# Kernel tuning notes

Measured on AMD Instinct MI355X. Metric: run time of the kernel, lower is better.

The kernel has to match this reference:

```python
import jax, jax.numpy as jnp
import numpy as np

V, B, C, H, W, D, G = 5, 1, 32, 384, 384, 4, 8


def _rot(a, b, c):
    ca, sa = np.cos(a), np.sin(a)
    cb, sb = np.cos(b), np.sin(b)
    cc, sc = np.cos(c), np.sin(c)
    Rx = np.array([[1, 0, 0], [0, ca, -sa], [0, sa, ca]])
    Ry = np.array([[cb, 0, sb], [0, 1, 0], [-sb, 0, cb]])
    Rz = np.array([[cc, -sc, 0], [sc, cc, 0], [0, 0, 1]])
    return (Rz @ Ry @ Rx).astype(np.float32)


def setup_inputs():
    key = jax.random.key(0)
    ks = jax.random.split(key, 8)
    features = jax.random.normal(ks[0], (V, B, C, H, W), jnp.float32)
    current_depths = jax.random.uniform(ks[1], (B, D, H, W), jnp.float32, 425.0, 935.0)
    rng = np.random.RandomState(0)
    Ks = np.zeros((B, V, 3, 3), np.float32)
    Es = np.zeros((B, V, 3, 4), np.float32)
    for b in range(B):
        for v in range(V):
            f = 0.8 * W * (1.0 + 0.01 * rng.randn())
            Ks[b, v] = np.array([[f, 0, W / 2.0], [0, f, H / 2.0], [0, 0, 1.0]], np.float32)
            if v == 0:
                Rm = np.eye(3, dtype=np.float32)
                t = np.zeros(3, np.float32)
            else:
                Rm = _rot(*(0.02 * rng.randn(3)))
                t = np.array([25.0 * v, 5.0 * rng.randn(), 5.0 * rng.randn()], np.float32)
            Es[b, v, :, :3] = Rm
            Es[b, v, :, 3] = t
    w0 = 0.3 * jax.random.normal(ks[2], (16, G), jnp.float32)
    b0 = jnp.zeros((16,), jnp.float32)
    w1 = 0.3 * jax.random.normal(ks[3], (8, 16), jnp.float32)
    b1 = jnp.zeros((8,), jnp.float32)
    w2 = 0.3 * jax.random.normal(ks[4], (1, 8), jnp.float32)
    b2 = jnp.zeros((1,), jnp.float32)
    return {"features": features, "current_depths": current_depths,
            "cam_intrinsic": jnp.asarray(Ks), "cam_extrinsic": jnp.asarray(Es),
            "w0": w0, "b0": b0, "w1": w1, "b1": b1, "w2": w2, "b2": b2}


def _bilinear_sample(feat, px, py):
    # feat [B,C,H,W]; px,py [B,N] pixel coords (align_corners=True), zero padding
    Bn, Cn, Hn, Wn = feat.shape
    ff = feat.reshape(Bn, Cn, Hn * Wn)
    x0 = jnp.floor(px)
    y0 = jnp.floor(py)
    wx1 = px - x0
    wx0 = 1.0 - wx1
    wy1 = py - y0
    wy0 = 1.0 - wy1

    def gather(xi, yi, w):
        valid = (xi >= 0) & (xi <= Wn - 1) & (yi >= 0) & (yi <= Hn - 1)
        xc = jnp.clip(xi, 0, Wn - 1).astype(jnp.int32)
        yc = jnp.clip(yi, 0, Hn - 1).astype(jnp.int32)
        idx = yc * Wn + xc  # [B,N]
        v = jnp.take_along_axis(ff, idx[:, None, :], axis=2)  # [B,C,N]
        return v * (w * valid)[:, None, :]

    return (gather(x0, y0, wx0 * wy0) + gather(x0 + 1.0, y0, wx1 * wy0)
            + gather(x0, y0 + 1.0, wx0 * wy1) + gather(x0 + 1.0, y0 + 1.0, wx1 * wy1))


def _pixelwise_net(sim, w0, b0, w1, b1, w2, b2):
    # PixelwiseNet: 1x1x1 Conv3d G->16->8->1 (BN folded to identity, eval stats), sigmoid, max over depth
    x = jax.nn.relu(jnp.einsum('og,bgdhw->bodhw', w0, sim) + b0[None, :, None, None, None])
    x = jax.nn.relu(jnp.einsum('oc,bcdhw->bodhw', w1, x) + b1[None, :, None, None, None])
    x = jnp.einsum('oc,bcdhw->bodhw', w2, x) + b2[None, :, None, None, None]
    return jnp.max(jax.nn.sigmoid(x), axis=2)  # [B,1,H,W]


def reference(features, current_depths, cam_intrinsic, cam_extrinsic, w0, b0, w1, b1, w2, b2):
    ref_feat = features[0]                                   # [B,C,H,W]
    ref_g = ref_feat.reshape(B, G, C // G, H, W)
    # pixel grid with half-pixel centers, homogeneous [3, H*W]
    xs = jnp.arange(W, dtype=jnp.float32) + 0.5
    ys = jnp.arange(H, dtype=jnp.float32) + 0.5
    gx, gy = jnp.meshgrid(xs, ys)                            # [H,W]
    grid = jnp.stack([gx.ravel(), gy.ravel(), jnp.ones(H * W, jnp.float32)], 0)
    K_ref_inv = jnp.linalg.inv(cam_intrinsic[:, 0])          # [B,3,3]
    R = cam_extrinsic[:, :, :3, :3]                          # [B,V,3,3]
    t = cam_extrinsic[:, :, :3, 3:4]                         # [B,V,3,1]
    R_ref_inv = jnp.linalg.inv(R[:, 0])                      # [B,3,3]
    uv = jnp.einsum('bij,jn->bin', K_ref_inv, grid)          # [B,3,HW]
    cam_pts = uv[:, None] * current_depths.reshape(B, D, 1, H * W)   # [B,D,3,HW]
    world = jnp.einsum('bij,bdjn->bdin', R_ref_inv, cam_pts - t[:, 0:1])
    world = world.transpose(0, 2, 1, 3).reshape(B, 3, D * H * W)     # [B,3,N], N=D*H*W
    sim_sum = 0.0
    w_sum = 0.0
    for s in range(1, V):
        cp = jnp.einsum('bij,bjn->bin', R[:, s], world) + t[:, s]    # [B,3,N]
        uvd = jnp.einsum('bij,bjn->bin', cam_intrinsic[:, s], cp)
        z = uvd[:, 2] + 1e-9
        px = uvd[:, 0] / z
        py = uvd[:, 1] / z
        warped = _bilinear_sample(features[s], px, py)               # [B,C,N]
        warped = warped.reshape(B, G, C // G, D, H, W)
        sim = jnp.mean(warped * ref_g[:, :, :, None], axis=2)        # [B,G,D,H,W]
        vw = _pixelwise_net(sim, w0, b0, w1, b1, w2, b2)             # [B,1,H,W]
        sim_sum = sim_sum + sim * vw[:, :, None]
        w_sum = w_sum + vw[:, :, None]
    return sim_sum / w_sum
```

## Files before the change

kernel.cpp:

```cpp
#include <hip/hip_runtime.h>
#include <math.h>

#define Vn 5
#define Cn 32
#define Hn 384
#define Wn 384
#define Dn 4
#define Gn 8
#define HWn (Hn*Wn)

typedef _Float16 h2 __attribute__((ext_vector_type(2)));
typedef float    f2 __attribute__((ext_vector_type(2)));

__device__ __forceinline__ float fdot2h(h2 a, h2 b, float c){
#if __has_builtin(__builtin_amdgcn_fdot2)
    return __builtin_amdgcn_fdot2(a, b, c, false);
#else
    return (float)a.x*(float)b.x + (float)a.y*(float)b.y + c;
#endif
}
__device__ __forceinline__ unsigned int packh2(float a, float b){
    h2 h;
    h.x = (_Float16)a;
    h.y = (_Float16)b;
    return __builtin_bit_cast(unsigned int, h);
}
__device__ __forceinline__ f2 fma2(f2 a, f2 b, f2 c){ return __builtin_elementwise_fma(a, b, c); }
__device__ __forceinline__ f2 max2(f2 a, f2 b){ return __builtin_elementwise_max(a, b); }
__device__ __forceinline__ f2 splat2(float x){ f2 r; r.x = x; r.y = x; return r; }

__device__ __forceinline__ void inv3(const float* m, float* o){
    float a=m[0],b=m[1],c=m[2],d=m[3],e=m[4],f=m[5],g=m[6],h=m[7],i=m[8];
    float A =  e*i - f*h;
    float B = -(d*i - f*g);
    float C =  d*h - e*g;
    float det = a*A + b*B + c*C;
    float r = 1.f/det;
    o[0] = A*r;            o[1] = -(b*i - c*h)*r;  o[2] =  (b*f - c*e)*r;
    o[3] = B*r;            o[4] =  (a*i - c*g)*r;  o[5] = -(a*f - c*d)*r;
    o[6] = C*r;            o[7] = -(a*h - b*g)*r;  o[8] =  (a*e - b*d)*r;
}
__device__ __forceinline__ void mm3(const float* a, const float* b, float* o){
    #pragma unroll
    for (int r=0;r<3;r++)
        #pragma unroll
        for (int c=0;c<3;c++)
            o[r*3+c] = a[r*3+0]*b[0*3+c] + a[r*3+1]*b[1*3+c] + a[r*3+2]*b[2*3+c];
}
__device__ __forceinline__ void mv3(const float* a, const float* v, float* o){
    #pragma unroll
    for (int r=0;r<3;r++)
        o[r] = a[r*3+0]*v[0] + a[r*3+1]*v[1] + a[r*3+2]*v[2];
}

__global__ __launch_bounds__(256)
void transpose_kernel(const float* __restrict__ feat, unsigned short* __restrict__ featT){
    const int s  = blockIdx.y;
    const int p0 = blockIdx.x * 1024 + threadIdx.x * 4;
    const float* src = feat + (size_t)(s+1)*Cn*HWn + p0;
    unsigned int outw[4][16];
    #pragma unroll
    for (int c=0; c<Cn; c+=2){
        const float4 a = *(const float4*)(src + (size_t)c*HWn);
        const float4 b = *(const float4*)(src + (size_t)(c+1)*HWn);
        outw[0][c>>1] = packh2(a.x, b.x);
        outw[1][c>>1] = packh2(a.y, b.y);
        outw[2][c>>1] = packh2(a.z, b.z);
        outw[3][c>>1] = packh2(a.w, b.w);
    }
    uint4* dst = (uint4*)(featT + ((size_t)s*HWn + p0)*Cn);
    #pragma unroll
    for (int p=0;p<4;p++){
        #pragma unroll
        for (int q=0;q<4;q++){
            uint4 o;
            o.x = outw[p][4*q+0];
            o.y = outw[p][4*q+1];
            o.z = outw[p][4*q+2];
            o.w = outw[p][4*q+3];
            dst[p*4+q] = o;
        }
    }
}

#define DOTG(uA, uB, g, WV)                                                    \
    {                                                                          \
        const h2 pa = __builtin_bit_cast(h2, (uA));                            \
        const h2 pb = __builtin_bit_cast(h2, (uB));                            \
        const float dt = fdot2h(pa, r2[2*(g)], fdot2h(pb, r2[2*(g)+1], 0.f));  \
        sg[(g)] = fmaf((WV), dt, sg[(g)]);                                     \
    }

__device__ __forceinline__ void tap_f16(const unsigned short* __restrict__ vbase,
                                        int xc, int yc, float w,
                                        const h2* r2, float* sg)
{
    if (w != 0.f){
        const uint4* p = (const uint4*)(vbase + ((size_t)yc*Wn + xc)*Cn);
        const uint4 q0 = p[0];
        const uint4 q1 = p[1];
        const uint4 q2 = p[2];
        const uint4 q3 = p[3];
        DOTG(q0.x, q0.y, 0, w)
        DOTG(q0.z, q0.w, 1, w)
        DOTG(q1.x, q1.y, 2, w)
        DOTG(q1.z, q1.w, 3, w)
        DOTG(q2.x, q2.y, 4, w)
        DOTG(q2.z, q2.w, 5, w)
        DOTG(q3.x, q3.y, 6, w)
        DOTG(q3.z, q3.w, 7, w)
    }
}

__global__ __launch_bounds__(256, 2)
void gbinet_kernel(const float* __restrict__ feat,
                   const float* __restrict__ depths,
                   const float* __restrict__ Kin,
                   const float* __restrict__ Ein,
                   const float* __restrict__ w0, const float* __restrict__ b0,
                   const float* __restrict__ w1, const float* __restrict__ b1,
                   const float* __restrict__ w2, const float* __restrict__ b2,
                   const unsigned short* __restrict__ featT,
                   float* __restrict__ out)
{
    __shared__ float sW0[128], sW1[128], sB0[16], sB1[8], sW2[8], sB2s[1];
    __shared__ float sM[48];
    __shared__ float sRef[64*33];
    __shared__ float sDep[4*65];
    __shared__ float sOut[64*33];
    const int t = threadIdx.x;
    if (t < 128){ sW0[t] = w0[t]; sW1[t] = w1[t]; }
    if (t < 16) sB0[t] = b0[t];
    if (t < 8){ sB1[t] = b1[t]; sW2[t] = w2[t]; }

    const int bid = blockIdx.x;
    const int sid = (bid & 7) * (HWn/64/8) + (bid >> 3);
    const int blockBase = sid * 64;

    {
        const float* srcR = feat + blockBase;
        #pragma unroll
        for (int k=0;k<8;k++){
            const int i  = k*256 + t;
            const int c  = i >> 6;
            const int px = i & 63;
            sRef[px*33 + c] = srcR[(size_t)c*HWn + px];
        }
        const int dp = t >> 6;
        const int px = t & 63;
        sDep[dp*65 + px] = depths[(size_t)dp*HWn + blockBase + px];
    }

    if (t < 4){
        float K0inv[9]; inv3(Kin, K0inv);
        float R0[9], t0[3];
        #pragma unroll
        for (int r=0;r<3;r++){
            #pragma unroll
            for (int c=0;c<3;c++) R0[r*3+c] = Ein[r*4+c];
            t0[r] = Ein[r*4+3];
        }
        float R0inv[9]; inv3(R0, R0inv);
        float M0[9]; mm3(R0inv, K0inv, M0);
        float Rt0[3]; mv3(R0inv, t0, Rt0);
        const int sv = t + 1;
        const float* Ks = Kin + sv*9;
        const float* Es = Ein + sv*12;
        float Rs[9], ts[3];
        #pragma unroll
        for (int r=0;r<3;r++){
            #pragma unroll
            for (int c=0;c<3;c++) Rs[r*3+c] = Es[r*4+c];
            ts[r] = Es[r*4+3];
        }
        float T1[9]; mm3(Rs, M0, T1);
        float A[9];  mm3(Ks, T1, A);
        float Rr[3]; mv3(Rs, Rt0, Rr);
        float tv[3] = { ts[0]-Rr[0], ts[1]-Rr[1], ts[2]-Rr[2] };
        float cv[3]; mv3(Ks, tv, cv);
        float* dm = &sM[t*12];
        #pragma unroll
        for (int i=0;i<9;i++) dm[i] = A[i];
        #pragma unroll
        for (int i=0;i<3;i++) dm[9+i] = cv[i];
    }
    if (t == 4) sB2s[0] = b2[0];
    __syncthreads();

    const int pixLocal = t >> 2;
    const int s        = t & 3;
    const int pix      = blockBase + pixLocal;
    const float xg = (float)(pix % Wn) + 0.5f;
    const float yg = (float)(pix / Wn) + 0.5f;

    h2 r2[16];
    #pragma unroll
    for (int k=0;k<16;k++){
        r2[k].x = (_Float16)sRef[pixLocal*33 + 2*k];
        r2[k].y = (_Float16)sRef[pixLocal*33 + 2*k+1];
    }
    float dep[Dn];
    #pragma unroll
    for (int d=0;d<Dn;d++) dep[d] = sDep[d*65 + pixLocal];

    const float* M = &sM[s*12];
    const float bx = M[0]*xg + M[1]*yg + M[2];
    const float by = M[3]*xg + M[4]*yg + M[5];
    const float bz = M[6]*xg + M[7]*yg + M[8];
    const float cx = M[9], cy = M[10], cz = M[11];
    const unsigned short* vbase = featT + (size_t)s*HWn*Cn;

    float sim[Gn][Dn];
    #pragma unroll
    for (int d=0;d<Dn;d++){
        const float dd = dep[d];
        const float ux = fmaf(bx, dd, cx);
        const float uy = fmaf(by, dd, cy);
        const float uz = fmaf(bz, dd, cz) + 1e-9f;
        const float rz = 1.f/uz;
        const float px = ux*rz, py = uy*rz;
        const float x0 = floorf(px), y0 = floorf(py);
        const float wx1 = px - x0, wy1 = py - y0;
        const float wx0 = 1.f - wx1, wy0 = 1.f - wy1;
        const bool vx0 = (x0 >= 0.f)     && (x0 <= (float)(Wn-1));
        const bool vx1 = (x0 >= -1.f)    && (x0 <= (float)(Wn-2));
        const bool vy0 = (y0 >= 0.f)     && (y0 <= (float)(Hn-1));
        const bool vy1 = (y0 >= -1.f)    && (y0 <= (float)(Hn-2));
        const float w00 = (vx0&&vy0) ? 0.25f*wx0*wy0 : 0.f;
        const float w10 = (vx1&&vy0) ? 0.25f*wx1*wy0 : 0.f;
        const float w01 = (vx0&&vy1) ? 0.25f*wx0*wy1 : 0.f;
        const float w11 = (vx1&&vy1) ? 0.25f*wx1*wy1 : 0.f;
        const int xi0 = (int)fminf(fmaxf(x0,     0.f), (float)(Wn-1));
        const int xi1 = (int)fminf(fmaxf(x0+1.f, 0.f), (float)(Wn-1));
        const int yi0 = (int)fminf(fmaxf(y0,     0.f), (float)(Hn-1));
        const int yi1 = (int)fminf(fmaxf(y0+1.f, 0.f), (float)(Hn-1));

        float sg[Gn];
        #pragma unroll
        for (int g=0; g<Gn; g++) sg[g] = 0.f;
        tap_f16(vbase, xi0, yi0, w00, r2, sg);
        tap_f16(vbase, xi1, yi0, w10, r2, sg);
        tap_f16(vbase, xi0, yi1, w01, r2, sg);
        tap_f16(vbase, xi1, yi1, w11, r2, sg);
        #pragma unroll
        for (int g=0; g<Gn; g++) sim[g][d] = sg[g];
    }

    float maxlog = -3.0e38f;
    #pragma unroll
    for (int dp=0; dp<2; dp++){
        const int d0 = 2*dp, d1 = 2*dp+1;
        f2 sv[Gn];
        #pragma unroll
        for (int g=0; g<Gn; g++){ sv[g].x = sim[g][d0]; sv[g].y = sim[g][d1]; }
        f2 h[16];
        #pragma unroll
        for (int o=0;o<16;o++){
            f2 a = splat2(sB0[o]);
            #pragma unroll
            for (int g=0; g<Gn; g++)
                a = fma2(splat2(sW0[o*Gn+g]), sv[g], a);
            h[o] = max2(a, splat2(0.f));
        }
        f2 lg = splat2(sB2s[0]);
        #pragma unroll
        for (int o=0;o<8;o++){
            f2 a = splat2(sB1[o]);
            #pragma unroll
            for (int i=0;i<16;i++)
                a = fma2(splat2(sW1[o*16+i]), h[i], a);
            lg = fma2(splat2(sW2[o]), max2(a, splat2(0.f)), lg);
        }
        maxlog = fmaxf(maxlog, fmaxf(lg.x, lg.y));
    }
    const float vw = 1.f/(1.f + __expf(-maxlog));

    float wsum = vw;
    wsum += __shfl_xor(wsum, 1);
    wsum += __shfl_xor(wsum, 2);
    #pragma unroll
    for (int g=0;g<Gn;g++)
        #pragma unroll
        for (int d=0;d<Dn;d++){
            float v = sim[g][d]*vw;
            v += __shfl_xor(v, 1);
            v += __shfl_xor(v, 2);
            sim[g][d] = v;
        }

    if (s == 0){
        const float invw = 1.f/wsum;
        #pragma unroll
        for (int g=0;g<Gn;g++)
            #pragma unroll
            for (int d=0;d<Dn;d++)
                sOut[pixLocal*33 + g*Dn + d] = sim[g][d]*invw;
    }
    __syncthreads();

    float* oBase = out + blockBase;
    #pragma unroll
    for (int k=0;k<8;k++){
        const int e     = k*256 + t;
        const int plane = e >> 6;
        const int pixel = e & 63;
        oBase[(size_t)plane*HWn + pixel] = sOut[pixel*33 + plane];
    }
}

extern "C" void kernel_launch(void* const* d_in, const int* in_sizes, int n_in,
                              void* d_out, int out_size, void* d_ws, size_t ws_size,
                              hipStream_t stream)
{
    (void)in_sizes; (void)n_in; (void)out_size; (void)ws_size;
    const float* feat   = (const float*)d_in[0];
    const float* depths = (const float*)d_in[1];
    const float* K      = (const float*)d_in[2];
    const float* E      = (const float*)d_in[3];
    const float* w0     = (const float*)d_in[4];
    const float* b0     = (const float*)d_in[5];
    const float* w1     = (const float*)d_in[6];
    const float* b1     = (const float*)d_in[7];
    const float* w2     = (const float*)d_in[8];
    const float* b2     = (const float*)d_in[9];
    float* out = (float*)d_out;
    unsigned short* featT = (unsigned short*)d_ws;

    dim3 g(HWn/1024, Vn-1);
    transpose_kernel<<<g, 256, 0, stream>>>(feat, featT);
    gbinet_kernel<<<HWn/64, 256, 0, stream>>>(feat, depths, K, E,
                                              w0,b0,w1,b1,w2,b2, featT, out);
}
```

Measured before the change: 244.1 us.

## Split depth hypotheses across thread pairs to double thread-level parallelism

Each (pixel, source view) pair is now handled by two threads, one per pair of depth hypotheses, instead of one thread covering all four depths. Blocks now cover 32 pixels instead of 64, and the grid is twice as large. The max over depth logits and the sums across views are done with adjusted shuffle patterns. The aim is fewer live registers per thread and more wavefronts in flight to hide the latency of the gather-heavy bilinear taps. The cost is duplicated per-thread setup: the reference-feature load, the projection base and the pixel-net weights are now read by twice as many threads.

```diff
diff --git a/kernel.cpp b/kernel.cpp
--- a/kernel.cpp
+++ b/kernel.cpp
@@ -125,30 +125,32 @@
 {
     __shared__ float sW0[128], sW1[128], sB0[16], sB1[8], sW2[8], sB2s[1];
     __shared__ float sM[48];
-    __shared__ float sRef[64*33];
-    __shared__ float sDep[4*65];
-    __shared__ float sOut[64*33];
+    __shared__ float sRef[32*33];
+    __shared__ float sDep[4*33];
+    __shared__ float sOut[32*33];
     const int t = threadIdx.x;
     if (t < 128){ sW0[t] = w0[t]; sW1[t] = w1[t]; }
     if (t < 16) sB0[t] = b0[t];
     if (t < 8){ sB1[t] = b1[t]; sW2[t] = w2[t]; }
 
     const int bid = blockIdx.x;
-    const int sid = (bid & 7) * (HWn/64/8) + (bid >> 3);
-    const int blockBase = sid * 64;
+    const int sid = (bid & 7) * (HWn/32/8) + (bid >> 3);
+    const int blockBase = sid * 32;
 
     {
         const float* srcR = feat + blockBase;
         #pragma unroll
-        for (int k=0;k<8;k++){
+        for (int k=0;k<4;k++){
             const int i  = k*256 + t;
-            const int c  = i >> 6;
-            const int px = i & 63;
+            const int c  = i >> 5;
+            const int px = i & 31;
             sRef[px*33 + c] = srcR[(size_t)c*HWn + px];
         }
-        const int dp = t >> 6;
-        const int px = t & 63;
-        sDep[dp*65 + px] = depths[(size_t)dp*HWn + blockBase + px];
+        if (t < 128){
+            const int dp = t >> 5;
+            const int px = t & 31;
+            sDep[dp*33 + px] = depths[(size_t)dp*HWn + blockBase + px];
+        }
     }
 
     if (t < 4){
@@ -187,8 +189,10 @@
     if (t == 4) sB2s[0] = b2[0];
     __syncthreads();
 
-    const int pixLocal = t >> 2;
-    const int s        = t & 3;
+    const int pixLocal = t >> 3;
+    const int sub      = t & 7;
+    const int s        = sub >> 1;
+    const int hh       = sub & 1;
     const int pix      = blockBase + pixLocal;
     const float xg = (float)(pix % Wn) + 0.5f;
     const float yg = (float)(pix / Wn) + 0.5f;
@@ -199,9 +203,9 @@
         r2[k].x = (_Float16)sRef[pixLocal*33 + 2*k];
         r2[k].y = (_Float16)sRef[pixLocal*33 + 2*k+1];
     }
-    float dep[Dn];
-    #pragma unroll
-    for (int d=0;d<Dn;d++) dep[d] = sDep[d*65 + pixLocal];
+    float dep[2];
+    #pragma unroll
+    for (int d=0;d<2;d++) dep[d] = sDep[(2*hh + d)*33 + pixLocal];
 
     const float* M = &sM[s*12];
     const float bx = M[0]*xg + M[1]*yg + M[2];
@@ -210,9 +214,9 @@
     const float cx = M[9], cy = M[10], cz = M[11];
     const unsigned short* vbase = featT + (size_t)s*HWn*Cn;
 
-    float sim[Gn][Dn];
-    #pragma unroll
-    for (int d=0;d<Dn;d++){
+    float sim[Gn][2];
+    #pragma unroll
+    for (int d=0;d<2;d++){
         const float dd = dep[d];
         const float ux = fmaf(bx, dd, cx);
         const float uy = fmaf(by, dd, cy);
@@ -246,45 +250,41 @@
         for (int g=0; g<Gn; g++) sim[g][d] = sg[g];
     }
 
-    float maxlog = -3.0e38f;
-    #pragma unroll
-    for (int dp=0; dp<2; dp++){
-        const int d0 = 2*dp, d1 = 2*dp+1;
-        f2 sv[Gn];
-        #pragma unroll
-        for (int g=0; g<Gn; g++){ sv[g].x = sim[g][d0]; sv[g].y = sim[g][d1]; }
-        f2 h[16];
-        #pragma unroll
-        for (int o=0;o<16;o++){
-            f2 a = splat2(sB0[o]);
-            #pragma unroll
-            for (int g=0; g<Gn; g++)
-                a = fma2(splat2(sW0[o*Gn+g]), sv[g], a);
-            h[o] = max2(a, splat2(0.f));
-        }
-        f2 lg = splat2(sB2s[0]);
-        #pragma unroll
-        for (int o=0;o<8;o++){
-            f2 a = splat2(sB1[o]);
-            #pragma unroll
-            for (int i=0;i<16;i++)
-                a = fma2(splat2(sW1[o*16+i]), h[i], a);
-            lg = fma2(splat2(sW2[o]), max2(a, splat2(0.f)), lg);
-        }
-        maxlog = fmaxf(maxlog, fmaxf(lg.x, lg.y));
-    }
+    f2 sv[Gn];
+    #pragma unroll
+    for (int g=0; g<Gn; g++){ sv[g].x = sim[g][0]; sv[g].y = sim[g][1]; }
+    f2 hreg[16];
+    #pragma unroll
+    for (int o=0;o<16;o++){
+        f2 a = splat2(sB0[o]);
+        #pragma unroll
+        for (int g=0; g<Gn; g++)
+            a = fma2(splat2(sW0[o*Gn+g]), sv[g], a);
+        hreg[o] = max2(a, splat2(0.f));
+    }
+    f2 lg = splat2(sB2s[0]);
+    #pragma unroll
+    for (int o=0;o<8;o++){
+        f2 a = splat2(sB1[o]);
+        #pragma unroll
+        for (int i=0;i<16;i++)
+            a = fma2(splat2(sW1[o*16+i]), hreg[i], a);
+        lg = fma2(splat2(sW2[o]), max2(a, splat2(0.f)), lg);
+    }
+    float mx = fmaxf(lg.x, lg.y);
+    const float maxlog = fmaxf(mx, __shfl_xor(mx, 1));
     const float vw = 1.f/(1.f + __expf(-maxlog));
 
     float wsum = vw;
-    wsum += __shfl_xor(wsum, 1);
     wsum += __shfl_xor(wsum, 2);
+    wsum += __shfl_xor(wsum, 4);
     #pragma unroll
     for (int g=0;g<Gn;g++)
         #pragma unroll
-        for (int d=0;d<Dn;d++){
+        for (int d=0;d<2;d++){
             float v = sim[g][d]*vw;
-            v += __shfl_xor(v, 1);
             v += __shfl_xor(v, 2);
+            v += __shfl_xor(v, 4);
             sim[g][d] = v;
         }
 
@@ -293,17 +293,17 @@
         #pragma unroll
         for (int g=0;g<Gn;g++)
             #pragma unroll
-            for (int d=0;d<Dn;d++)
-                sOut[pixLocal*33 + g*Dn + d] = sim[g][d]*invw;
+            for (int d=0;d<2;d++)
+                sOut[pixLocal*33 + g*Dn + 2*hh + d] = sim[g][d]*invw;
     }
     __syncthreads();
 
     float* oBase = out + blockBase;
     #pragma unroll
-    for (int k=0;k<8;k++){
+    for (int k=0;k<4;k++){
         const int e     = k*256 + t;
-        const int plane = e >> 6;
-        const int pixel = e & 63;
+        const int plane = e >> 5;
+        const int pixel = e & 31;
         oBase[(size_t)plane*HWn + pixel] = sOut[pixel*33 + plane];
     }
 }
@@ -328,6 +328,6 @@
 
     dim3 g(HWn/1024, Vn-1);
     transpose_kernel<<<g, 256, 0, stream>>>(feat, featT);
-    gbinet_kernel<<<HWn/64, 256, 0, stream>>>(feat, depths, K, E,
+    gbinet_kernel<<<HWn/32, 256, 0, stream>>>(feat, depths, K, E,
                                               w0,b0,w1,b1,w2,b2, featT, out);
 }
```

Result: no change. 242.4 us (-0.7%).

## Split channel quarters across lanes and transpose partial sums via shuffles

Applied to the files above, without the earlier changes.

Each of the four lanes per pixel used to handle one source view and load all 32 channels (64 bytes) per bilinear tap. Now each lane handles one 8-channel quarter across all four views with a single 16-byte load per tap, and the per-view partial dot products are redistributed with a butterfly of xor shuffles. As a result, the four lanes of a pixel read adjacent 16-byte slices of the same texel in each load instruction, which should coalesce better and lower register pressure from the reference vector. The cost is that every lane now does the projection math for all four views, and the transpose adds extra shuffle traffic.

```diff
diff --git a/kernel.cpp b/kernel.cpp
--- a/kernel.cpp
+++ b/kernel.cpp
@@ -83,32 +83,18 @@
     }
 }
 
-#define DOTG(uA, uB, g, WV)                                                    \
-    {                                                                          \
-        const h2 pa = __builtin_bit_cast(h2, (uA));                            \
-        const h2 pb = __builtin_bit_cast(h2, (uB));                            \
-        const float dt = fdot2h(pa, r2[2*(g)], fdot2h(pb, r2[2*(g)+1], 0.f));  \
-        sg[(g)] = fmaf((WV), dt, sg[(g)]);                                     \
-    }
-
-__device__ __forceinline__ void tap_f16(const unsigned short* __restrict__ vbase,
-                                        int xc, int yc, float w,
-                                        const h2* r2, float* sg)
+__device__ __forceinline__ void qtap(const unsigned short* __restrict__ vb,
+                                     int xc, int yc, float w,
+                                     const h2* r2q, float& sg0, float& sg1)
 {
     if (w != 0.f){
-        const uint4* p = (const uint4*)(vbase + ((size_t)yc*Wn + xc)*Cn);
-        const uint4 q0 = p[0];
-        const uint4 q1 = p[1];
-        const uint4 q2 = p[2];
-        const uint4 q3 = p[3];
-        DOTG(q0.x, q0.y, 0, w)
-        DOTG(q0.z, q0.w, 1, w)
-        DOTG(q1.x, q1.y, 2, w)
-        DOTG(q1.z, q1.w, 3, w)
-        DOTG(q2.x, q2.y, 4, w)
-        DOTG(q2.z, q2.w, 5, w)
-        DOTG(q3.x, q3.y, 6, w)
-        DOTG(q3.z, q3.w, 7, w)
+        const uint4 u = *(const uint4*)(vb + ((size_t)yc*Wn + xc)*Cn);
+        const h2 a0 = __builtin_bit_cast(h2, u.x);
+        const h2 a1 = __builtin_bit_cast(h2, u.y);
+        const h2 a2 = __builtin_bit_cast(h2, u.z);
+        const h2 a3 = __builtin_bit_cast(h2, u.w);
+        sg0 = fmaf(w, fdot2h(a0, r2q[0], fdot2h(a1, r2q[1], 0.f)), sg0);
+        sg1 = fmaf(w, fdot2h(a2, r2q[2], fdot2h(a3, r2q[3], 0.f)), sg1);
     }
 }
 
@@ -174,13 +160,13 @@
             ts[r] = Es[r*4+3];
         }
         float T1[9]; mm3(Rs, M0, T1);
-        float A[9];  mm3(Ks, T1, A);
+        float A9[9]; mm3(Ks, T1, A9);
         float Rr[3]; mv3(Rs, Rt0, Rr);
         float tv[3] = { ts[0]-Rr[0], ts[1]-Rr[1], ts[2]-Rr[2] };
         float cv[3]; mv3(Ks, tv, cv);
         float* dm = &sM[t*12];
         #pragma unroll
-        for (int i=0;i<9;i++) dm[i] = A[i];
+        for (int i=0;i<9;i++) dm[i] = A9[i];
         #pragma unroll
         for (int i=0;i<3;i++) dm[9+i] = cv[i];
     }
@@ -188,62 +174,93 @@
     __syncthreads();
 
     const int pixLocal = t >> 2;
-    const int s        = t & 3;
+    const int q        = t & 3;
     const int pix      = blockBase + pixLocal;
     const float xg = (float)(pix % Wn) + 0.5f;
     const float yg = (float)(pix / Wn) + 0.5f;
 
-    h2 r2[16];
-    #pragma unroll
-    for (int k=0;k<16;k++){
-        r2[k].x = (_Float16)sRef[pixLocal*33 + 2*k];
-        r2[k].y = (_Float16)sRef[pixLocal*33 + 2*k+1];
+    h2 r2q[4];
+    #pragma unroll
+    for (int k=0;k<4;k++){
+        r2q[k].x = (_Float16)sRef[pixLocal*33 + 8*q + 2*k];
+        r2q[k].y = (_Float16)sRef[pixLocal*33 + 8*q + 2*k+1];
     }
     float dep[Dn];
     #pragma unroll
     for (int d=0;d<Dn;d++) dep[d] = sDep[d*65 + pixLocal];
 
-    const float* M = &sM[s*12];
-    const float bx = M[0]*xg + M[1]*yg + M[2];
-    const float by = M[3]*xg + M[4]*yg + M[5];
-    const float bz = M[6]*xg + M[7]*yg + M[8];
-    const float cx = M[9], cy = M[10], cz = M[11];
-    const unsigned short* vbase = featT + (size_t)s*HWn*Cn;
-
-    float sim[Gn][Dn];
-    #pragma unroll
-    for (int d=0;d<Dn;d++){
-        const float dd = dep[d];
-        const float ux = fmaf(bx, dd, cx);
-        const float uy = fmaf(by, dd, cy);
-        const float uz = fmaf(bz, dd, cz) + 1e-9f;
-        const float rz = 1.f/uz;
-        const float px = ux*rz, py = uy*rz;
-        const float x0 = floorf(px), y0 = floorf(py);
-        const float wx1 = px - x0, wy1 = py - y0;
-        const float wx0 = 1.f - wx1, wy0 = 1.f - wy1;
-        const bool vx0 = (x0 >= 0.f)     && (x0 <= (float)(Wn-1));
-        const bool vx1 = (x0 >= -1.f)    && (x0 <= (float)(Wn-2));
-        const bool vy0 = (y0 >= 0.f)     && (y0 <= (float)(Hn-1));
-        const bool vy1 = (y0 >= -1.f)    && (y0 <= (float)(Hn-2));
-        const float w00 = (vx0&&vy0) ? 0.25f*wx0*wy0 : 0.f;
-        const float w10 = (vx1&&vy0) ? 0.25f*wx1*wy0 : 0.f;
-        const float w01 = (vx0&&vy1) ? 0.25f*wx0*wy1 : 0.f;
-        const float w11 = (vx1&&vy1) ? 0.25f*wx1*wy1 : 0.f;
-        const int xi0 = (int)fminf(fmaxf(x0,     0.f), (float)(Wn-1));
-        const int xi1 = (int)fminf(fmaxf(x0+1.f, 0.f), (float)(Wn-1));
-        const int yi0 = (int)fminf(fmaxf(y0,     0.f), (float)(Hn-1));
-        const int yi1 = (int)fminf(fmaxf(y0+1.f, 0.f), (float)(Hn-1));
-
-        float sg[Gn];
-        #pragma unroll
-        for (int g=0; g<Gn; g++) sg[g] = 0.f;
-        tap_f16(vbase, xi0, yi0, w00, r2, sg);
-        tap_f16(vbase, xi1, yi0, w10, r2, sg);
-        tap_f16(vbase, xi0, yi1, w01, r2, sg);
-        tap_f16(vbase, xi1, yi1, w11, r2, sg);
-        #pragma unroll
-        for (int g=0; g<Gn; g++) sim[g][d] = sg[g];
+    float A[4][8];
+    #pragma unroll
+    for (int v=0;v<4;v++)
+        #pragma unroll
+        for (int i=0;i<8;i++) A[v][i] = 0.f;
+
+    #pragma unroll
+    for (int v=0; v<4; v++){
+        const float* M = &sM[v*12];
+        const float bx = M[0]*xg + M[1]*yg + M[2];
+        const float by = M[3]*xg + M[4]*yg + M[5];
+        const float bz = M[6]*xg + M[7]*yg + M[8];
+        const float cx = M[9], cy = M[10], cz = M[11];
+        const unsigned short* vbase = featT + (size_t)v*HWn*Cn + q*8;
+        #pragma unroll
+        for (int d=0; d<Dn; d++){
+            const float dd = dep[d];
+            const float ux = fmaf(bx, dd, cx);
+            const float uy = fmaf(by, dd, cy);
+            const float uz = fmaf(bz, dd, cz) + 1e-9f;
+            const float rz = 1.f/uz;
+            const float px = ux*rz, py = uy*rz;
+            const float x0 = floorf(px), y0 = floorf(py);
+            const float wx1 = px - x0, wy1 = py - y0;
+            const float wx0 = 1.f - wx1, wy0 = 1.f - wy1;
+            const bool vx0 = (x0 >= 0.f)     && (x0 <= (float)(Wn-1));
+            const bool vx1 = (x0 >= -1.f)    && (x0 <= (float)(Wn-2));
+            const bool vy0 = (y0 >= 0.f)     && (y0 <= (float)(Hn-1));
+            const bool vy1 = (y0 >= -1.f)    && (y0 <= (float)(Hn-2));
+            const float w00 = (vx0&&vy0) ? 0.25f*wx0*wy0 : 0.f;
+            const float w10 = (vx1&&vy0) ? 0.25f*wx1*wy0 : 0.f;
+            const float w01 = (vx0&&vy1) ? 0.25f*wx0*wy1 : 0.f;
+            const float w11 = (vx1&&vy1) ? 0.25f*wx1*wy1 : 0.f;
+            const int xi0 = (int)fminf(fmaxf(x0,     0.f), (float)(Wn-1));
+            const int xi1 = (int)fminf(fmaxf(x0+1.f, 0.f), (float)(Wn-1));
+            const int yi0 = (int)fminf(fmaxf(y0,     0.f), (float)(Hn-1));
+            const int yi1 = (int)fminf(fmaxf(y0+1.f, 0.f), (float)(Hn-1));
+
+            float sg0 = 0.f, sg1 = 0.f;
+            qtap(vbase, xi0, yi0, w00, r2q, sg0, sg1);
+            qtap(vbase, xi1, yi0, w10, r2q, sg0, sg1);
+            qtap(vbase, xi0, yi1, w01, r2q, sg0, sg1);
+            qtap(vbase, xi1, yi1, w11, r2q, sg0, sg1);
+            A[v][d]   = sg0;
+            A[v][4+d] = sg1;
+        }
+    }
+
+    const bool q0b = (q & 1) != 0;
+    const bool q1b = (q & 2) != 0;
+    float Bp[2][2][8];
+    #pragma unroll
+    for (int i=0;i<8;i++){
+        const float s0 = q0b ? A[0][i] : A[1][i];
+        const float s1 = q0b ? A[2][i] : A[3][i];
+        const float r0 = __shfl_xor(s0, 1);
+        const float r1 = __shfl_xor(s1, 1);
+        Bp[0][0][i] = q0b ? r0 : A[0][i];
+        Bp[0][1][i] = q0b ? A[1][i] : r0;
+        Bp[1][0][i] = q0b ? r1 : A[2][i];
+        Bp[1][1][i] = q0b ? A[3][i] : r1;
+    }
+    float Cp[2][2][8];
+    #pragma unroll
+    for (int i=0;i<8;i++){
+        #pragma unroll
+        for (int g0=0; g0<2; g0++){
+            const float tt = q1b ? Bp[0][g0][i] : Bp[1][g0][i];
+            const float u  = __shfl_xor(tt, 2);
+            Cp[0][g0][i] = q1b ? u : Bp[0][g0][i];
+            Cp[1][g0][i] = q1b ? Bp[1][g0][i] : u;
+        }
     }
 
     float maxlog = -3.0e38f;
@@ -252,15 +269,18 @@
         const int d0 = 2*dp, d1 = 2*dp+1;
         f2 sv[Gn];
         #pragma unroll
-        for (int g=0; g<Gn; g++){ sv[g].x = sim[g][d0]; sv[g].y = sim[g][d1]; }
-        f2 h[16];
+        for (int g=0; g<Gn; g++){
+            sv[g].x = Cp[g>>2][(g>>1)&1][(g&1)*4 + d0];
+            sv[g].y = Cp[g>>2][(g>>1)&1][(g&1)*4 + d1];
+        }
+        f2 hreg[16];
         #pragma unroll
         for (int o=0;o<16;o++){
             f2 a = splat2(sB0[o]);
             #pragma unroll
             for (int g=0; g<Gn; g++)
                 a = fma2(splat2(sW0[o*Gn+g]), sv[g], a);
-            h[o] = max2(a, splat2(0.f));
+            hreg[o] = max2(a, splat2(0.f));
         }
         f2 lg = splat2(sB2s[0]);
         #pragma unroll
@@ -268,7 +288,7 @@
             f2 a = splat2(sB1[o]);
             #pragma unroll
             for (int i=0;i<16;i++)
-                a = fma2(splat2(sW1[o*16+i]), h[i], a);
+                a = fma2(splat2(sW1[o*16+i]), hreg[i], a);
             lg = fma2(splat2(sW2[o]), max2(a, splat2(0.f)), lg);
         }
         maxlog = fmaxf(maxlog, fmaxf(lg.x, lg.y));
@@ -279,22 +299,24 @@
     wsum += __shfl_xor(wsum, 1);
     wsum += __shfl_xor(wsum, 2);
     #pragma unroll
-    for (int g=0;g<Gn;g++)
-        #pragma unroll
-        for (int d=0;d<Dn;d++){
-            float v = sim[g][d]*vw;
-            v += __shfl_xor(v, 1);
-            v += __shfl_xor(v, 2);
-            sim[g][d] = v;
-        }
-
-    if (s == 0){
+    for (int j1=0;j1<2;j1++)
+        #pragma unroll
+        for (int j0=0;j0<2;j0++)
+            #pragma unroll
+            for (int i=0;i<8;i++){
+                float vv = Cp[j1][j0][i]*vw;
+                vv += __shfl_xor(vv, 1);
+                vv += __shfl_xor(vv, 2);
+                Cp[j1][j0][i] = vv;
+            }
+
+    if (q == 0){
         const float invw = 1.f/wsum;
         #pragma unroll
         for (int g=0;g<Gn;g++)
             #pragma unroll
             for (int d=0;d<Dn;d++)
-                sOut[pixLocal*33 + g*Dn + d] = sim[g][d]*invw;
+                sOut[pixLocal*33 + g*Dn + d] = Cp[g>>2][(g>>1)&1][(g&1)*4+d]*invw;
     }
     __syncthreads();
 
```

Measured after the change: 259.6 us. 6.4% more time.
